# Performance work log

Measured on AMD Instinct MI355X. Metric: run time of the kernel, lower is better.

## Reference

```python
import jax, jax.numpy as jnp
import numpy as np

N_NODES = 50000
N_EDGES = 600000
DIM = 128
HEADS = 8
HEAD_DIM = DIM // HEADS  # 16


def leaky(x, slope=0.01):
    return jnp.where(x >= 0, x, slope * x)


def gat_layer(x, W, a_src, a_dst, bias, src, dst):
    # x: [N, DIM]; W: [DIM, DIM]; a_src/a_dst: [HEADS, HEAD_DIM]; bias: [DIM]
    N = x.shape[0]
    xh = (x @ W).reshape(N, HEADS, HEAD_DIM)
    alpha_src = jnp.sum(xh * a_src, axis=-1)  # [N, H]
    alpha_dst = jnp.sum(xh * a_dst, axis=-1)  # [N, H]
    e = leaky(alpha_src[src] + alpha_dst[dst], 0.2)  # [E, H], PyG negative_slope=0.2
    # segment softmax over edges sharing the same destination node
    e_max = jax.ops.segment_max(e, dst, num_segments=N)
    ex = jnp.exp(e - e_max[dst])
    denom = jax.ops.segment_sum(ex, dst, num_segments=N)
    alpha = ex / (denom[dst] + 1e-16)
    out = jax.ops.segment_sum(xh[src] * alpha[:, :, None], dst, num_segments=N)
    return out.reshape(N, DIM) + bias


def setup_inputs() -> dict:
    key = jax.random.key(0)
    ks = jax.random.split(key, 20)
    s_d = 1.0 / np.sqrt(DIM)
    s_h = 1.0 / np.sqrt(DIM // 2)
    inp = {
        'features': jax.random.normal(ks[0], (N_NODES, DIM), jnp.float32),
        'edge_index': jax.random.randint(ks[1], (2, N_EDGES), 0, N_NODES, jnp.int64)
            if jax.config.jax_enable_x64 else
            jax.random.randint(ks[1], (2, N_EDGES), 0, N_NODES).astype(jnp.int32),
        'W1': jax.random.normal(ks[2], (DIM, DIM), jnp.float32) * s_d,
        'a_src1': jax.random.normal(ks[3], (HEADS, HEAD_DIM), jnp.float32) * s_d,
        'a_dst1': jax.random.normal(ks[4], (HEADS, HEAD_DIM), jnp.float32) * s_d,
        'b1': jnp.zeros((DIM,), jnp.float32),
        'W2': jax.random.normal(ks[5], (DIM, DIM), jnp.float32) * s_d,
        'a_src2': jax.random.normal(ks[6], (HEADS, HEAD_DIM), jnp.float32) * s_d,
        'a_dst2': jax.random.normal(ks[7], (HEADS, HEAD_DIM), jnp.float32) * s_d,
        'b2': jnp.zeros((DIM,), jnp.float32),
        'wm1': jax.random.normal(ks[8], (DIM, DIM // 2), jnp.float32) * s_d,
        'bm1': jnp.zeros((DIM // 2,), jnp.float32),
        'wm2': jax.random.normal(ks[9], (DIM // 2, 1), jnp.float32) * s_h,
        'bm2': jnp.zeros((1,), jnp.float32),
        'wa1': jax.random.normal(ks[10], (DIM, DIM // 2), jnp.float32) * s_d,
        'ba1': jnp.zeros((DIM // 2,), jnp.float32),
        'wa2': jax.random.normal(ks[11], (DIM // 2, DIM), jnp.float32) * s_h,
        'ba2': jnp.zeros((DIM,), jnp.float32),
        'gamma': jnp.ones((DIM,), jnp.float32),
        'beta': jnp.zeros((DIM,), jnp.float32),
    }
    return inp


def reference(features, edge_index, W1, a_src1, a_dst1, b1, W2, a_src2, a_dst2, b2,
              wm1, bm1, wm2, bm2, wa1, ba1, wa2, ba2, gamma, beta):
    N = features.shape[0]
    loops = jnp.arange(N, dtype=edge_index.dtype)
    src = jnp.concatenate([edge_index[0], loops])  # PyG add_self_loops=True
    dst = jnp.concatenate([edge_index[1], loops])
    h = leaky(gat_layer(features, W1, a_src1, a_dst1, b1, src, dst))
    h = leaky(gat_layer(h, W2, a_src2, a_dst2, b2, src, dst))
    scores = (leaky(h @ wm1 + bm1) @ wm2 + bm2)[:, 0]  # [N]
    w = jax.nn.softmax(scores, axis=0)
    agg = jnp.sum(w[:, None] * h, axis=0)  # [DIM]
    z = leaky(agg @ wa1 + ba1) @ wa2 + ba2
    mu = jnp.mean(z)
    var = jnp.mean((z - mu) ** 2)
    return gamma * (z - mu) / jnp.sqrt(var + 1e-5) + beta
```

## Files before the change

kernel.cpp:

```cpp
#include <hip/hip_runtime.h>
#include <math.h>

#define DIM 128
#define HEADS 8
#define HD 16
#define CAP 64

typedef __attribute__((ext_vector_type(8))) short s16x8;
typedef __attribute__((ext_vector_type(8))) unsigned short u16x8;
typedef __attribute__((ext_vector_type(4))) float f32x4;

__device__ __forceinline__ float lrelu(float x, float s) { return x >= 0.f ? x : s * x; }

__device__ __forceinline__ unsigned short f2bf(float x) {
  unsigned u = __float_as_uint(x);
  return (unsigned short)((u + 0x7FFFu + ((u >> 16) & 1u)) >> 16);
}
__device__ __forceinline__ float bf2f(unsigned short b) {
  return __uint_as_float(((unsigned)b) << 16);
}

__global__ __launch_bounds__(256) void k_scan_blk(const int* __restrict__ cnt, int n,
                                                  int* __restrict__ excl, int* __restrict__ bsum) {
  __shared__ int wsum[4];
  int tid = threadIdx.x, l = tid & 63, w = tid >> 6;
  int i = blockIdx.x * 256 + tid;
  int v = (i < n) ? cnt[i] : 0;
  int s = v;
#pragma unroll
  for (int off = 1; off < 64; off <<= 1) {
    int t = __shfl_up(s, off, 64);
    if (l >= off) s += t;
  }
  if (l == 63) wsum[w] = s;
  __syncthreads();
  int add = 0;
#pragma unroll
  for (int k = 0; k < 4; ++k) add += (k < w) ? wsum[k] : 0;
  if (i < n) excl[i] = s + add - v;
  if (tid == 255) bsum[blockIdx.x] = s + add;
}

__global__ __launch_bounds__(256) void k_scan_top(const int* __restrict__ bsum, int nb,
                                                  int* __restrict__ boff, int* __restrict__ rowptrN) {
  __shared__ int wsum[4];
  int tid = threadIdx.x, l = tid & 63, w = tid >> 6;
  int v = (tid < nb) ? bsum[tid] : 0;
  int s = v;
#pragma unroll
  for (int off = 1; off < 64; off <<= 1) {
    int t = __shfl_up(s, off, 64);
    if (l >= off) s += t;
  }
  if (l == 63) wsum[w] = s;
  __syncthreads();
  int add = 0;
#pragma unroll
  for (int k = 0; k < 4; ++k) add += (k < w) ? wsum[k] : 0;
  if (tid < nb) boff[tid] = s + add - v;
  if (tid == 255) *rowptrN = s + add;
}

__global__ __launch_bounds__(256) void k_scan_fix(int* __restrict__ cursor, const int* __restrict__ boff,
                                                  int n, int* __restrict__ rowptr) {
  int i = blockIdx.x * 256 + threadIdx.x;
  if (i < n) {
    int r = boff[blockIdx.x] + cursor[i];
    rowptr[i] = r;
    cursor[i] = r;
  }
}

__global__ void k_scatter(const int* __restrict__ ei, int E, int N,
                          int* __restrict__ cursor, int* __restrict__ colb) {
  int tot = E + N;
  for (int i = blockIdx.x * blockDim.x + threadIdx.x; i < tot; i += gridDim.x * blockDim.x) {
    int s, d;
    if (i < E) { s = ei[i]; d = ei[E + i]; } else { s = i - E; d = s; }
    int pos = atomicAdd(&cursor[d], 1);
    colb[pos] = s;
  }
}

__global__ __launch_bounds__(256) void k_prep(
    const float* __restrict__ W1, const float* __restrict__ as1, const float* __restrict__ ad1,
    const float* __restrict__ W2, const float* __restrict__ as2, const float* __restrict__ ad2,
    const float* __restrict__ wm1,
    unsigned short* __restrict__ wh1,
    unsigned short* __restrict__ sh1, unsigned short* __restrict__ sl1,
    unsigned short* __restrict__ wh2,
    unsigned short* __restrict__ sh2, unsigned short* __restrict__ sl2,
    unsigned short* __restrict__ mh, unsigned short* __restrict__ ml,
    int* __restrict__ cnt, int N) {
  int b = blockIdx.x, tid = threadIdx.x;
  if (b < 32) {
    int layer = b >> 4;
    const float* W = layer ? W2 : W1;
    unsigned short* wh = layer ? wh2 : wh1;
    int lo = (b & 15) * 1024;
    for (int idx = lo + tid; idx < lo + 1024; idx += 256) {
      int n = idx >> 7, k = idx & 127;
      wh[idx] = f2bf(W[k * DIM + n]);
    }
  } else if (b < 36) {
    int layer = (b - 32) >> 1;
    const float* W = layer ? W2 : W1;
    const float* avs = layer ? as2 : as1;
    const float* avd = layer ? ad2 : ad1;
    unsigned short* sh = layer ? sh2 : sh1;
    unsigned short* sl = layer ? sl2 : sl1;
    int lo = ((b - 32) & 1) * 1024;
    for (int idx = lo + tid; idx < lo + 1024; idx += 256) {
      int n = idx >> 7, k = idx & 127;
      float acc = 0.f;
      if (n < 8) {
#pragma unroll
        for (int j = 0; j < 16; ++j) acc += W[k * DIM + n * 16 + j] * avs[n * 16 + j];
      } else {
        int h = n - 8;
#pragma unroll
        for (int j = 0; j < 16; ++j) acc += W[k * DIM + h * 16 + j] * avd[h * 16 + j];
      }
      unsigned short hb = f2bf(acc);
      sh[idx] = hb;
      sl[idx] = f2bf(acc - bf2f(hb));
    }
  } else if (b < 44) {
    int lo = (b - 36) * 1024;
    for (int idx = lo + tid; idx < lo + 1024; idx += 256) {
      int j = idx >> 7, k = idx & 127;
      float v = wm1[k * 64 + j];
      unsigned short hb = f2bf(v);
      mh[idx] = hb;
      ml[idx] = f2bf(v - bf2f(hb));
    }
  } else {
    int i0 = (b - 44) * 2048 + tid * 8;
    if (i0 + 8 <= N) {
      int4 z = {0, 0, 0, 0};
      *(int4*)(cnt + i0) = z;
      *(int4*)(cnt + i0 + 4) = z;
    } else {
      for (int i = i0; i < N; ++i) cnt[i] = 0;
    }
  }
}

template <int BF16IN, int FUSEHIST>
__global__ __launch_bounds__(256) void k_linear_mfma(
    const void* __restrict__ xin,
    const unsigned short* __restrict__ wh,
    const unsigned short* __restrict__ sh, const unsigned short* __restrict__ sl,
    unsigned short* __restrict__ xhb, float* __restrict__ asrc, float* __restrict__ adst,
    int N, int GL,
    const int* __restrict__ ei, int E, int* __restrict__ cnt) {
  if constexpr (FUSEHIST) {
    if ((int)blockIdx.x >= GL) {
      int tot = E + N;
      int nhb = gridDim.x - GL;
      for (int i = ((int)blockIdx.x - GL) * 256 + (int)threadIdx.x; i < tot; i += nhb * 256) {
        int d = (i < E) ? ei[E + i] : (i - E);
        atomicAdd(&cnt[d], 1);
      }
      return;
    }
  }
  __shared__ unsigned short tile[64][136];
  __shared__ float atile[64][16];
  int tid = threadIdx.x, l = tid & 63, w = tid >> 6;
  int g = l >> 4, c = l & 15;
  int t0 = w * 2, t1 = t0 + 1;
  int rb = blockIdx.x * 64;

  const s16x8* Bh = (const s16x8*)wh;
  const s16x8* Shp = (const s16x8*)sh;
  const s16x8* Slp = (const s16x8*)sl;
  s16x8 B0[4], B1[4], S0[4], S1[4];
#pragma unroll
  for (int kt = 0; kt < 4; ++kt) {
    B0[kt] = Bh[(t0 * 16 + c) * 16 + kt * 4 + g];
    B1[kt] = Bh[(t1 * 16 + c) * 16 + kt * 4 + g];
    S0[kt] = Shp[c * 16 + kt * 4 + g];
    S1[kt] = Slp[c * 16 + kt * 4 + g];
  }

  s16x8 A[4][4];
#pragma unroll
  for (int q = 0; q < 4; ++q) {
    int rc = min(rb + q * 16 + c, N - 1);
    if constexpr (BF16IN) {
      const s16x8* xr = (const s16x8*)((const unsigned short*)xin + (size_t)rc * DIM);
#pragma unroll
      for (int kt = 0; kt < 4; ++kt) A[q][kt] = xr[kt * 4 + g];
    } else {
      const float4* xf = (const float4*)((const float*)xin + (size_t)rc * DIM);
#pragma unroll
      for (int kt = 0; kt < 4; ++kt) {
        float4 p = xf[kt * 8 + g * 2];
        float4 qq = xf[kt * 8 + g * 2 + 1];
        s16x8 a;
        a[0] = (short)f2bf(p.x); a[1] = (short)f2bf(p.y);
        a[2] = (short)f2bf(p.z); a[3] = (short)f2bf(p.w);
        a[4] = (short)f2bf(qq.x); a[5] = (short)f2bf(qq.y);
        a[6] = (short)f2bf(qq.z); a[7] = (short)f2bf(qq.w);
        A[q][kt] = a;
      }
    }
  }

  f32x4 acc[4][2];
#pragma unroll
  for (int q = 0; q < 4; ++q) {
    acc[q][0] = (f32x4){0.f, 0.f, 0.f, 0.f};
    acc[q][1] = (f32x4){0.f, 0.f, 0.f, 0.f};
  }
#pragma unroll
  for (int kt = 0; kt < 4; ++kt)
#pragma unroll
    for (int q = 0; q < 4; ++q) {
      acc[q][0] = __builtin_amdgcn_mfma_f32_16x16x32_bf16(A[q][kt], B0[kt], acc[q][0], 0, 0, 0);
      acc[q][1] = __builtin_amdgcn_mfma_f32_16x16x32_bf16(A[q][kt], B1[kt], acc[q][1], 0, 0, 0);
    }
  f32x4 accS = {0.f, 0.f, 0.f, 0.f};
#pragma unroll
  for (int kt = 0; kt < 4; ++kt) {
    accS = __builtin_amdgcn_mfma_f32_16x16x32_bf16(A[w][kt], S0[kt], accS, 0, 0, 0);
    accS = __builtin_amdgcn_mfma_f32_16x16x32_bf16(A[w][kt], S1[kt], accS, 0, 0, 0);
  }

#pragma unroll
  for (int q = 0; q < 4; ++q)
#pragma unroll
    for (int r = 0; r < 4; ++r) {
      tile[q * 16 + g * 4 + r][t0 * 16 + c] = f2bf(acc[q][0][r]);
      tile[q * 16 + g * 4 + r][t1 * 16 + c] = f2bf(acc[q][1][r]);
    }
#pragma unroll
  for (int r = 0; r < 4; ++r) atile[w * 16 + g * 4 + r][c] = accS[r];
  __syncthreads();

#pragma unroll
  for (int p = 0; p < 4; ++p) {
    int row = p * 16 + (tid >> 4), cb = tid & 15;
    int rr = rb + row;
    if (rr < N) {
      u16x8 v = *(const u16x8*)&tile[row][cb * 8];
      *(u16x8*)(xhb + (size_t)rr * DIM + cb * 8) = v;
      float av = atile[row][cb];
      if (cb < 8) asrc[rr * HEADS + cb] = av;
      else adst[rr * HEADS + (cb - 8)] = av;
    }
  }
}

__global__ __launch_bounds__(256) void k_gat_agg(const int* __restrict__ rowptr, const int* __restrict__ colb,
                                                 const unsigned short* __restrict__ xhb,
                                                 const float* __restrict__ asrc, const float* __restrict__ adst,
                                                 const float* __restrict__ bias,
                                                 unsigned short* __restrict__ houtb, int N) {
  __shared__ int ci[4][CAP];
  int tid = threadIdx.x, lane = tid & 63, wv = tid >> 6;
  int n = blockIdx.x * 4 + wv;
  int base = 0, deg = 0;
  if (n < N) { base = rowptr[n]; deg = rowptr[n + 1] - base; }
  if (lane < deg && lane < CAP) ci[wv][lane] = colb[base + lane];
  __syncthreads();
  if (n >= N) return;

  int qt = lane >> 4, q = lane & 15;
  int h = q >> 1;
  float adn = adst[n * HEADS + h];
  float den = 0.f;
  float a0 = 0.f, a1 = 0.f, a2 = 0.f, a3 = 0.f, a4 = 0.f, a5 = 0.f, a6 = 0.f, a7 = 0.f;
#define EDGE(ii) { \
    int c_ = ((ii) < CAP) ? ci[wv][(ii)] : colb[base + (ii)]; \
    float e_ = lrelu(asrc[c_ * HEADS + h] + adn, 0.2f); \
    float w_ = __expf(e_); \
    den += w_; \
    u16x8 u_ = *(const u16x8*)(xhb + (size_t)c_ * DIM + q * 8); \
    a0 = fmaf(w_, bf2f((unsigned short)u_[0]), a0); \
    a1 = fmaf(w_, bf2f((unsigned short)u_[1]), a1); \
    a2 = fmaf(w_, bf2f((unsigned short)u_[2]), a2); \
    a3 = fmaf(w_, bf2f((unsigned short)u_[3]), a3); \
    a4 = fmaf(w_, bf2f((unsigned short)u_[4]), a4); \
    a5 = fmaf(w_, bf2f((unsigned short)u_[5]), a5); \
    a6 = fmaf(w_, bf2f((unsigned short)u_[6]), a6); \
    a7 = fmaf(w_, bf2f((unsigned short)u_[7]), a7); }
  int i = qt;
  for (; i + 4 < deg; i += 8) { EDGE(i); EDGE(i + 4); }
  for (; i < deg; i += 4) { EDGE(i); }
#undef EDGE
  den += __shfl_xor(den, 16, 64); den += __shfl_xor(den, 32, 64);
  a0 += __shfl_xor(a0, 16, 64); a0 += __shfl_xor(a0, 32, 64);
  a1 += __shfl_xor(a1, 16, 64); a1 += __shfl_xor(a1, 32, 64);
  a2 += __shfl_xor(a2, 16, 64); a2 += __shfl_xor(a2, 32, 64);
  a3 += __shfl_xor(a3, 16, 64); a3 += __shfl_xor(a3, 32, 64);
  a4 += __shfl_xor(a4, 16, 64); a4 += __shfl_xor(a4, 32, 64);
  a5 += __shfl_xor(a5, 16, 64); a5 += __shfl_xor(a5, 32, 64);
  a6 += __shfl_xor(a6, 16, 64); a6 += __shfl_xor(a6, 32, 64);
  a7 += __shfl_xor(a7, 16, 64); a7 += __shfl_xor(a7, 32, 64);
  if (qt == 0) {
    float r = 1.f / (den + 1e-16f);
    const float4* bp = (const float4*)(bias + q * 8);
    float4 b0 = bp[0], b1 = bp[1];
    u16x8 o;
    o[0] = f2bf(lrelu(fmaf(a0, r, b0.x), 0.01f));
    o[1] = f2bf(lrelu(fmaf(a1, r, b0.y), 0.01f));
    o[2] = f2bf(lrelu(fmaf(a2, r, b0.z), 0.01f));
    o[3] = f2bf(lrelu(fmaf(a3, r, b0.w), 0.01f));
    o[4] = f2bf(lrelu(fmaf(a4, r, b1.x), 0.01f));
    o[5] = f2bf(lrelu(fmaf(a5, r, b1.y), 0.01f));
    o[6] = f2bf(lrelu(fmaf(a6, r, b1.z), 0.01f));
    o[7] = f2bf(lrelu(fmaf(a7, r, b1.w), 0.01f));
    *(u16x8*)(houtb + (size_t)n * DIM + q * 8) = o;
  }
}

__global__ __launch_bounds__(256) void k_score_pool(
    const unsigned short* __restrict__ h2b,
    const unsigned short* __restrict__ mh, const unsigned short* __restrict__ ml,
    const float* __restrict__ bm1, const float* __restrict__ wm2, const float* __restrict__ bm2,
    float* __restrict__ pagg, float* __restrict__ psum, int N) {
  __shared__ float se[4][16];
  __shared__ float blkacc[4][128];
  __shared__ float swave[4];
  int tid = threadIdx.x, l = tid & 63, w = tid >> 6;
  int g = l >> 4, c = l & 15;
  int rbase = blockIdx.x * 64 + w * 16;
  int rc = min(rbase + c, N - 1);
  const s16x8* xr = (const s16x8*)(h2b + (size_t)rc * DIM);
  s16x8 A[4];
#pragma unroll
  for (int kt = 0; kt < 4; ++kt) A[kt] = xr[kt * 4 + g];

  const s16x8* Bh = (const s16x8*)mh;
  const s16x8* Bl = (const s16x8*)ml;
  float v[4] = {0.f, 0.f, 0.f, 0.f};
#pragma unroll
  for (int ct = 0; ct < 4; ++ct) {
    f32x4 acc = {0.f, 0.f, 0.f, 0.f};
#pragma unroll
    for (int kt = 0; kt < 4; ++kt) {
      s16x8 bh = Bh[(ct * 16 + c) * 16 + kt * 4 + g];
      s16x8 bl = Bl[(ct * 16 + c) * 16 + kt * 4 + g];
      acc = __builtin_amdgcn_mfma_f32_16x16x32_bf16(A[kt], bh, acc, 0, 0, 0);
      acc = __builtin_amdgcn_mfma_f32_16x16x32_bf16(A[kt], bl, acc, 0, 0, 0);
    }
    int col = ct * 16 + c;
    float b = bm1[col], w2 = wm2[col];
#pragma unroll
    for (int r = 0; r < 4; ++r) v[r] += lrelu(acc[r] + b, 0.01f) * w2;
  }
#pragma unroll
  for (int r = 0; r < 4; ++r) {
    v[r] += __shfl_xor(v[r], 1, 64);
    v[r] += __shfl_xor(v[r], 2, 64);
    v[r] += __shfl_xor(v[r], 4, 64);
    v[r] += __shfl_xor(v[r], 8, 64);
  }
  float b2 = bm2[0];
  float e[4];
#pragma unroll
  for (int r = 0; r < 4; ++r) {
    int rr = rbase + g * 4 + r;
    e[r] = (rr < N) ? __expf(v[r] + b2) : 0.f;
  }
  if (c == 0) {
#pragma unroll
    for (int r = 0; r < 4; ++r) se[w][g * 4 + r] = e[r];
  }
  __syncthreads();
  float emy = se[w][c];
  float pa[32];
#pragma unroll
  for (int kt = 0; kt < 4; ++kt)
#pragma unroll
    for (int j = 0; j < 8; ++j)
      pa[kt * 8 + j] = emy * bf2f((unsigned short)A[kt][j]);
#pragma unroll
  for (int k = 0; k < 32; ++k) {
    pa[k] += __shfl_xor(pa[k], 1, 64);
    pa[k] += __shfl_xor(pa[k], 2, 64);
    pa[k] += __shfl_xor(pa[k], 4, 64);
    pa[k] += __shfl_xor(pa[k], 8, 64);
  }
  if (c == 0) {
#pragma unroll
    for (int kt = 0; kt < 4; ++kt)
#pragma unroll
      for (int j = 0; j < 8; ++j)
        blkacc[w][kt * 32 + g * 8 + j] = pa[kt * 8 + j];
  }
  float ws = e[0] + e[1] + e[2] + e[3];
  ws += __shfl_xor(ws, 16, 64);
  ws += __shfl_xor(ws, 32, 64);
  if (l == 0) swave[w] = ws;
  __syncthreads();
  if (tid < 128) {
    float s = blkacc[0][tid] + blkacc[1][tid] + blkacc[2][tid] + blkacc[3][tid];
    pagg[(size_t)blockIdx.x * DIM + tid] = s;
  }
  if (tid == 0) psum[blockIdx.x] = swave[0] + swave[1] + swave[2] + swave[3];
}

__global__ __launch_bounds__(1024) void k_final(const float* __restrict__ psum, const float* __restrict__ pagg,
                                                int nb,
                                                const float* __restrict__ wa1, const float* __restrict__ ba1,
                                                const float* __restrict__ wa2, const float* __restrict__ ba2,
                                                const float* __restrict__ gamma, const float* __restrict__ beta,
                                                float* __restrict__ out) {
  __shared__ float redz[1024];
  __shared__ float reda[8][128];
  __shared__ float sa[128], shh[64], red[128];
  int t = threadIdx.x;
  float zp = 0.f;
  for (int b = t; b < nb; b += 1024) zp += psum[b];
  redz[t] = zp;
  __syncthreads();
  for (int st = 512; st > 0; st >>= 1) { if (t < st) redz[t] += redz[t + st]; __syncthreads(); }
  int d = t & 127, g = t >> 7;
  float ag = 0.f;
  for (int b = g; b < nb; b += 8) ag += pagg[(size_t)b * DIM + d];
  reda[g][d] = ag;
  __syncthreads();
  if (g == 0) {
    float s = 0.f;
#pragma unroll
    for (int k = 0; k < 8; ++k) s += reda[k][d];
    sa[d] = s / redz[0];
  }
  __syncthreads();
  if (t < 64) {
    float a = 0.f;
    for (int k = 0; k < 128; ++k) a = fmaf(sa[k], wa1[k * 64 + t], a);
    a += ba1[t];
    shh[t] = lrelu(a, 0.01f);
  }
  __syncthreads();
  float zval = 0.f;
  if (t < 128) {
    zval = ba2[t];
    for (int j = 0; j < 64; ++j) zval = fmaf(shh[j], wa2[j * 128 + t], zval);
    red[t] = zval;
  }
  __syncthreads();
  for (int st = 64; st > 0; st >>= 1) { if (t < st) red[t] += red[t + st]; __syncthreads(); }
  float mu = red[0] / 128.f;
  __syncthreads();
  if (t < 128) red[t] = (zval - mu) * (zval - mu);
  __syncthreads();
  for (int st = 64; st > 0; st >>= 1) { if (t < st) red[t] += red[t + st]; __syncthreads(); }
  float var = red[0] / 128.f;
  if (t < 128) out[t] = gamma[t] * (zval - mu) / sqrtf(var + 1e-5f) + beta[t];
}

extern "C" void kernel_launch(void* const* d_in, const int* in_sizes, int n_in,
                              void* d_out, int out_size, void* d_ws, size_t ws_size,
                              hipStream_t stream) {
  const float* feat = (const float*)d_in[0];
  const int* ei = (const int*)d_in[1];
  const float* W1 = (const float*)d_in[2];
  const float* as1 = (const float*)d_in[3];
  const float* ad1 = (const float*)d_in[4];
  const float* b1 = (const float*)d_in[5];
  const float* W2 = (const float*)d_in[6];
  const float* as2 = (const float*)d_in[7];
  const float* ad2 = (const float*)d_in[8];
  const float* b2 = (const float*)d_in[9];
  const float* wm1 = (const float*)d_in[10];
  const float* bm1 = (const float*)d_in[11];
  const float* wm2 = (const float*)d_in[12];
  const float* bm2 = (const float*)d_in[13];
  const float* wa1 = (const float*)d_in[14];
  const float* ba1 = (const float*)d_in[15];
  const float* wa2 = (const float*)d_in[16];
  const float* ba2 = (const float*)d_in[17];
  const float* gamma = (const float*)d_in[18];
  const float* beta = (const float*)d_in[19];
  float* out = (float*)d_out;

  int N = in_sizes[0] / DIM;
  int E = in_sizes[1] / 2;
  int NB = (N + 255) / 256;
  int ZB = (N + 2047) / 2048;
  int GL = (N + 63) / 64;
  int GH = 448;
  int gs = (N + 63) / 64;

  char* ws = (char*)d_ws;
  size_t off = 0;
  auto alloc = [&](size_t bytes) -> void* {
    void* p = ws + off;
    off = (off + bytes + 255) & ~(size_t)255;
    return p;
  };
  int* cnt = (int*)alloc((size_t)N * 4);
  int* rowptr = (int*)alloc((size_t)(N + 1) * 4);
  int* cursor = (int*)alloc((size_t)N * 4);
  int* colb = (int*)alloc((size_t)(E + N) * 4);
  unsigned short* xhb = (unsigned short*)alloc((size_t)N * DIM * 2);
  unsigned short* h1b = (unsigned short*)alloc((size_t)N * DIM * 2);
  unsigned short* h2b = (unsigned short*)alloc((size_t)N * DIM * 2);
  float* asrcb = (float*)alloc((size_t)N * HEADS * 4);
  float* adstb = (float*)alloc((size_t)N * HEADS * 4);
  float* pagg = (float*)alloc((size_t)gs * DIM * 4);
  float* psum = (float*)alloc((size_t)gs * 4);
  int* bsum = (int*)alloc((size_t)NB * 4);
  int* boff = (int*)alloc((size_t)NB * 4);
  unsigned short* wh1 = (unsigned short*)alloc(DIM * DIM * 2);
  unsigned short* sh1 = (unsigned short*)alloc(16 * DIM * 2);
  unsigned short* sl1 = (unsigned short*)alloc(16 * DIM * 2);
  unsigned short* wh2 = (unsigned short*)alloc(DIM * DIM * 2);
  unsigned short* sh2 = (unsigned short*)alloc(16 * DIM * 2);
  unsigned short* sl2 = (unsigned short*)alloc(16 * DIM * 2);
  unsigned short* mh = (unsigned short*)alloc(64 * DIM * 2);
  unsigned short* ml = (unsigned short*)alloc(64 * DIM * 2);

  k_prep<<<44 + ZB, 256, 0, stream>>>(W1, as1, ad1, W2, as2, ad2, wm1,
                                      wh1, sh1, sl1, wh2, sh2, sl2, mh, ml, cnt, N);

  k_linear_mfma<0, 1><<<GL + GH, 256, 0, stream>>>(feat, wh1, sh1, sl1, xhb, asrcb, adstb,
                                                   N, GL, ei, E, cnt);

  k_scan_blk<<<NB, 256, 0, stream>>>(cnt, N, cursor, bsum);
  k_scan_top<<<1, 256, 0, stream>>>(bsum, NB, boff, rowptr + N);
  k_scan_fix<<<NB, 256, 0, stream>>>(cursor, boff, N, rowptr);
  k_scatter<<<1024, 256, 0, stream>>>(ei, E, N, cursor, colb);

  int ga = (N + 3) / 4;
  k_gat_agg<<<ga, 256, 0, stream>>>(rowptr, colb, xhb, asrcb, adstb, b1, h1b, N);
  k_linear_mfma<1, 0><<<GL, 256, 0, stream>>>(h1b, wh2, sh2, sl2, xhb, asrcb, adstb,
                                              N, GL, nullptr, 0, nullptr);
  k_gat_agg<<<ga, 256, 0, stream>>>(rowptr, colb, xhb, asrcb, adstb, b2, h2b, N);

  k_score_pool<<<gs, 256, 0, stream>>>(h2b, mh, ml, bm1, wm2, bm2, pagg, psum, N);
  k_final<<<1, 1024, 0, stream>>>(psum, pagg, gs, wa1, ba1, wa2, ba2, gamma, beta, out);
}
```

Measured before the change: 243.7 us.

## Stage weights in LDS and give each wave one row block across all columns

The linear MFMA kernel now copies the full bf16 weight matrix and the two score-projection matrices into shared memory. Each wave then loads only its own 16 rows of activations and computes all 8 column tiles, reading B fragments from LDS. Before, every wave loaded all 64 rows of activations, so each row was read from global memory four times per block. The change removes that redundant activation traffic at the cost of about 43 KB of LDS for staging weights, a block-wide barrier, and extra LDS reads, which may lower occupancy.

Result: faster. 223.5 us, median of 2 (-8.3%).

```diff
diff --git a/kernel.cpp b/kernel.cpp
--- a/kernel.cpp
+++ b/kernel.cpp
@@ -165,76 +165,70 @@
       return;
     }
   }
-  __shared__ unsigned short tile[64][136];
+  __shared__ unsigned short sB[160][136];
+  __shared__ unsigned short otile[64][136];
   __shared__ float atile[64][16];
   int tid = threadIdx.x, l = tid & 63, w = tid >> 6;
   int g = l >> 4, c = l & 15;
-  int t0 = w * 2, t1 = t0 + 1;
   int rb = blockIdx.x * 64;
 
-  const s16x8* Bh = (const s16x8*)wh;
-  const s16x8* Shp = (const s16x8*)sh;
-  const s16x8* Slp = (const s16x8*)sl;
-  s16x8 B0[4], B1[4], S0[4], S1[4];
+  for (int i = tid; i < 160 * 16; i += 256) {
+    int row = i >> 4, c8 = i & 15;
+    u16x8 v;
+    if (row < 128) v = *(const u16x8*)(wh + row * 128 + c8 * 8);
+    else if (row < 144) v = *(const u16x8*)(sh + (row - 128) * 128 + c8 * 8);
+    else v = *(const u16x8*)(sl + (row - 144) * 128 + c8 * 8);
+    *(u16x8*)&sB[row][c8 * 8] = v;
+  }
+
+  int rc = min(rb + w * 16 + c, N - 1);
+  s16x8 A[4];
+  if constexpr (BF16IN) {
+    const s16x8* xr = (const s16x8*)((const unsigned short*)xin + (size_t)rc * DIM);
+#pragma unroll
+    for (int kt = 0; kt < 4; ++kt) A[kt] = xr[kt * 4 + g];
+  } else {
+    const float4* xf = (const float4*)((const float*)xin + (size_t)rc * DIM);
+#pragma unroll
+    for (int kt = 0; kt < 4; ++kt) {
+      float4 p = xf[kt * 8 + g * 2];
+      float4 q = xf[kt * 8 + g * 2 + 1];
+      s16x8 a;
+      a[0] = (short)f2bf(p.x); a[1] = (short)f2bf(p.y);
+      a[2] = (short)f2bf(p.z); a[3] = (short)f2bf(p.w);
+      a[4] = (short)f2bf(q.x); a[5] = (short)f2bf(q.y);
+      a[6] = (short)f2bf(q.z); a[7] = (short)f2bf(q.w);
+      A[kt] = a;
+    }
+  }
+  __syncthreads();
+
+  f32x4 acc[8];
+#pragma unroll
+  for (int ct = 0; ct < 8; ++ct) acc[ct] = (f32x4){0.f, 0.f, 0.f, 0.f};
 #pragma unroll
   for (int kt = 0; kt < 4; ++kt) {
-    B0[kt] = Bh[(t0 * 16 + c) * 16 + kt * 4 + g];
-    B1[kt] = Bh[(t1 * 16 + c) * 16 + kt * 4 + g];
-    S0[kt] = Shp[c * 16 + kt * 4 + g];
-    S1[kt] = Slp[c * 16 + kt * 4 + g];
-  }
-
-  s16x8 A[4][4];
-#pragma unroll
-  for (int q = 0; q < 4; ++q) {
-    int rc = min(rb + q * 16 + c, N - 1);
-    if constexpr (BF16IN) {
-      const s16x8* xr = (const s16x8*)((const unsigned short*)xin + (size_t)rc * DIM);
-#pragma unroll
-      for (int kt = 0; kt < 4; ++kt) A[q][kt] = xr[kt * 4 + g];
-    } else {
-      const float4* xf = (const float4*)((const float*)xin + (size_t)rc * DIM);
-#pragma unroll
-      for (int kt = 0; kt < 4; ++kt) {
-        float4 p = xf[kt * 8 + g * 2];
-        float4 qq = xf[kt * 8 + g * 2 + 1];
-        s16x8 a;
-        a[0] = (short)f2bf(p.x); a[1] = (short)f2bf(p.y);
-        a[2] = (short)f2bf(p.z); a[3] = (short)f2bf(p.w);
-        a[4] = (short)f2bf(qq.x); a[5] = (short)f2bf(qq.y);
-        a[6] = (short)f2bf(qq.z); a[7] = (short)f2bf(qq.w);
-        A[q][kt] = a;
-      }
-    }
-  }
-
-  f32x4 acc[4][2];
-#pragma unroll
-  for (int q = 0; q < 4; ++q) {
-    acc[q][0] = (f32x4){0.f, 0.f, 0.f, 0.f};
-    acc[q][1] = (f32x4){0.f, 0.f, 0.f, 0.f};
-  }
-#pragma unroll
-  for (int kt = 0; kt < 4; ++kt)
-#pragma unroll
-    for (int q = 0; q < 4; ++q) {
-      acc[q][0] = __builtin_amdgcn_mfma_f32_16x16x32_bf16(A[q][kt], B0[kt], acc[q][0], 0, 0, 0);
-      acc[q][1] = __builtin_amdgcn_mfma_f32_16x16x32_bf16(A[q][kt], B1[kt], acc[q][1], 0, 0, 0);
-    }
+    s16x8 a = A[kt];
+#pragma unroll
+    for (int ct = 0; ct < 8; ++ct) {
+      s16x8 b = *(const s16x8*)&sB[ct * 16 + c][kt * 32 + g * 8];
+      acc[ct] = __builtin_amdgcn_mfma_f32_16x16x32_bf16(a, b, acc[ct], 0, 0, 0);
+    }
+  }
   f32x4 accS = {0.f, 0.f, 0.f, 0.f};
 #pragma unroll
   for (int kt = 0; kt < 4; ++kt) {
-    accS = __builtin_amdgcn_mfma_f32_16x16x32_bf16(A[w][kt], S0[kt], accS, 0, 0, 0);
-    accS = __builtin_amdgcn_mfma_f32_16x16x32_bf16(A[w][kt], S1[kt], accS, 0, 0, 0);
-  }
-
-#pragma unroll
-  for (int q = 0; q < 4; ++q)
-#pragma unroll
-    for (int r = 0; r < 4; ++r) {
-      tile[q * 16 + g * 4 + r][t0 * 16 + c] = f2bf(acc[q][0][r]);
-      tile[q * 16 + g * 4 + r][t1 * 16 + c] = f2bf(acc[q][1][r]);
-    }
+    s16x8 shi = *(const s16x8*)&sB[128 + c][kt * 32 + g * 8];
+    s16x8 slo = *(const s16x8*)&sB[144 + c][kt * 32 + g * 8];
+    accS = __builtin_amdgcn_mfma_f32_16x16x32_bf16(A[kt], shi, accS, 0, 0, 0);
+    accS = __builtin_amdgcn_mfma_f32_16x16x32_bf16(A[kt], slo, accS, 0, 0, 0);
+  }
+
+#pragma unroll
+  for (int ct = 0; ct < 8; ++ct)
+#pragma unroll
+    for (int r = 0; r < 4; ++r)
+      otile[w * 16 + g * 4 + r][ct * 16 + c] = f2bf(acc[ct][r]);
 #pragma unroll
   for (int r = 0; r < 4; ++r) atile[w * 16 + g * 4 + r][c] = accS[r];
   __syncthreads();
@@ -244,7 +238,7 @@
     int row = p * 16 + (tid >> 4), cb = tid & 15;
     int rr = rb + row;
     if (rr < N) {
-      u16x8 v = *(const u16x8*)&tile[row][cb * 8];
+      u16x8 v = *(const u16x8*)&otile[row][cb * 8];
       *(u16x8*)(xhb + (size_t)rr * DIM + cb * 8) = v;
       float av = atile[row][cb];
       if (cb < 8) asrc[rr * HEADS + cb] = av;
```
